# Performance work log

Measured on AMD Instinct MI355X. Metric: run time of the kernel, lower is better.

Reference implementation:

```python
import jax, jax.numpy as jnp
import numpy as np

B, DIM, NX, NY = 4, 64, 256, 256
HEADS, DIM_HEAD, LATENT, DIM_OUT, KM = 4, 32, 128, 64, 2
DH = DIM_HEAD * KM  # LowRankKernel head dim (also RoPE dim) = 64
EPS = 1e-5
MIN_FREQ = 1.0 / 64.0  # RotaryEmbedding default in FactFormer/LNS repo


def _gelu(x):
    return jax.nn.gelu(x, approximate=False)  # torch nn.GELU default (erf)


def _conv1x1(u, w):
    # u: [b,c,h,w], w: [out,c]  (1x1 conv == channel matmul)
    return jnp.einsum('bchw,oc->bohw', u, w)


def _pooling_reducer(x, win, ln_g, ln_b, w1, w2, b2):
    # x: [b, n_keep, n_pool, c] -> Linear, mean-pool over n_pool, LN+FFN
    h = jnp.einsum('bnmc,hc->bnmh', x, win).mean(axis=2)  # [b, n, hid]
    m = h.mean(axis=-1, keepdims=True)
    v = h.var(axis=-1, keepdims=True)
    h = (h - m) / jnp.sqrt(v + EPS) * ln_g + ln_b
    return _gelu(h @ w1.T) @ w2.T + b2  # [b, n, latent]


def _rope_freqs(n):
    pos = jnp.linspace(0.0, 1.0, n) / MIN_FREQ  # scale/min_freq = 64
    inv = 1.0 / (10000.0 ** (jnp.arange(0, DH, 2, dtype=jnp.float32) / DH))
    f = pos[:, None] * inv[None, :]            # [n, DH//2]
    return jnp.concatenate([f, f], axis=-1)    # [n, DH]


def _apply_rope(x, f):
    # rotate_half = cat(-x2, x1) on half-split (FactFormer convention)
    d = x.shape[-1] // 2
    rot = jnp.concatenate([-x[..., d:], x[..., :d]], axis=-1)
    return x * jnp.cos(f) + rot * jnp.sin(f)


def _low_rank_kernel(x, wqk):
    # x: [b, n, latent] -> K: [b, heads, n, n]; scaling=1, dropout=Identity, qk_norm=False
    b, n, _ = x.shape
    qk = x @ wqk.T
    q, k = jnp.split(qk, 2, axis=-1)
    q = q.reshape(b, n, HEADS, DH).transpose(0, 2, 1, 3)
    k = k.reshape(b, n, HEADS, DH).transpose(0, 2, 1, 3)
    f = _rope_freqs(n)
    q = _apply_rope(q, f)
    k = _apply_rope(k, f)
    return jnp.einsum('bhid,bhjd->bhij', q, k)


def _forward(u, gn_w, gn_b, w_in_proj, w_to_in,
             px_win, px_ln_g, px_ln_b, px_w1, px_w2, px_b2,
             py_win, py_ln_g, py_ln_b, py_w1, py_w2, py_b2,
             kx_wqk, ky_wqk, out_w1, out_w2):
    # GroupNorm(1, dim): normalize over (C,H,W) per sample, affine
    m = u.mean(axis=(1, 2, 3), keepdims=True)
    v = u.var(axis=(1, 2, 3), keepdims=True)
    un = (u - m) / jnp.sqrt(v + EPS) * gn_w[None, :, None, None] + gn_b[None, :, None, None]
    u_phi = _conv1x1(un, w_in_proj)  # [b, heads*dim_head, nx, ny]
    ui = _conv1x1(un, w_to_in)       # [b, dim, nx, ny]
    # to_x: pool over ny -> tokens along nx; to_y: pool over nx -> tokens along ny
    ux = _pooling_reducer(ui.transpose(0, 2, 3, 1), px_win, px_ln_g, px_ln_b, px_w1, px_w2, px_b2)  # [b, nx, latent]
    uy = _pooling_reducer(ui.transpose(0, 3, 2, 1), py_win, py_ln_g, py_ln_b, py_w1, py_w2, py_b2)  # [b, ny, latent]
    kx = _low_rank_kernel(ux, kx_wqk)  # [b, h, nx, nx]
    ky = _low_rank_kernel(uy, ky_wqk)  # [b, h, ny, ny]
    b, hc, nx, ny = u_phi.shape
    up = u_phi.reshape(b, HEADS, hc // HEADS, nx, ny)
    up = jnp.einsum('bhij,bhcjm->bhcim', kx, up)
    up = jnp.einsum('bhlm,bhcim->bhcil', ky, up)
    up = up.reshape(b, hc, nx, ny)
    # InstanceNorm2d (no affine, no running stats)
    m2 = up.mean(axis=(2, 3), keepdims=True)
    v2 = up.var(axis=(2, 3), keepdims=True)
    upn = (up - m2) / jnp.sqrt(v2 + EPS)
    out = _conv1x1(_gelu(_conv1x1(upn, out_w1)), out_w2)
    return out + u


def setup_inputs() -> dict:
    key = jax.random.key(0)
    ks = jax.random.split(key, 16)
    def w(k, shape, s=0.02):
        return (jax.random.normal(k, shape) * s).astype(jnp.float32)
    return {
        'u': jax.random.normal(ks[0], (B, DIM, NX, NY), dtype=jnp.float32),
        'gn_w': jnp.ones((DIM,), jnp.float32), 'gn_b': jnp.zeros((DIM,), jnp.float32),
        'w_in_proj': w(ks[1], (HEADS * DIM_HEAD, DIM)),
        'w_to_in': w(ks[2], (DIM, DIM)),
        'px_win': w(ks[3], (DIM, DIM)),
        'px_ln_g': jnp.ones((DIM,), jnp.float32), 'px_ln_b': jnp.zeros((DIM,), jnp.float32),
        'px_w1': w(ks[4], (2 * DIM, DIM)), 'px_w2': w(ks[5], (LATENT, 2 * DIM)),
        'px_b2': jnp.zeros((LATENT,), jnp.float32),
        'py_win': w(ks[6], (DIM, DIM)),
        'py_ln_g': jnp.ones((DIM,), jnp.float32), 'py_ln_b': jnp.zeros((DIM,), jnp.float32),
        'py_w1': w(ks[7], (2 * DIM, DIM)), 'py_w2': w(ks[8], (LATENT, 2 * DIM)),
        'py_b2': jnp.zeros((LATENT,), jnp.float32),
        'kx_wqk': w(ks[9], (2 * HEADS * DH, LATENT)),
        'ky_wqk': w(ks[10], (2 * HEADS * DH, LATENT)),
        'out_w1': w(ks[11], (DIM_OUT, HEADS * DIM_HEAD)),
        'out_w2': w(ks[12], (DIM_OUT, DIM_OUT)),
    }


def reference(u, gn_w, gn_b, w_in_proj, w_to_in,
              px_win, px_ln_g, px_ln_b, px_w1, px_w2, px_b2,
              py_win, py_ln_g, py_ln_b, py_w1, py_w2, py_b2,
              kx_wqk, ky_wqk, out_w1, out_w2):
    return _forward(u, gn_w, gn_b, w_in_proj, w_to_in,
                    px_win, px_ln_g, px_ln_b, px_w1, px_w2, px_b2,
                    py_win, py_ln_g, py_ln_b, py_w1, py_w2, py_b2,
                    kx_wqk, ky_wqk, out_w1, out_w2)
```

## Files before the change

### kernel.cpp

```cpp
#include <hip/hip_runtime.h>
#include <math.h>

typedef unsigned short ushort_t;
typedef unsigned int uint_t;
typedef __attribute__((ext_vector_type(8))) short s8v;
typedef __attribute__((ext_vector_type(4))) float f4;

#define NPIX 65536
#define EPS_ 1e-5f

__device__ __forceinline__ float bf2f(ushort_t u){ return __uint_as_float(((uint_t)u)<<16); }
__device__ __forceinline__ ushort_t f2bf(float f){
  uint_t u = __float_as_uint(f);
  uint_t r = (u + 0x7fffu + ((u>>16)&1u)) >> 16;
  return (ushort_t)r;
}
__device__ __forceinline__ float bflo(uint_t p){ return __uint_as_float(p<<16); }
__device__ __forceinline__ float bfhi(uint_t p){ return __uint_as_float(p & 0xffff0000u); }
__device__ __forceinline__ uint_t packbf(float a, float b){ return (uint_t)f2bf(a) | ((uint_t)f2bf(b)<<16); }

__device__ __forceinline__ f4 MFMA(s8v a, s8v b, f4 c){
  return __builtin_amdgcn_mfma_f32_16x16x32_bf16(a, b, c, 0, 0, 0);
}

__device__ __forceinline__ float wave_sum(float v){
  #pragma unroll
  for(int m=32;m>=1;m>>=1) v += __shfl_xor(v, m, 64);
  return v;
}

__global__ __launch_bounds__(256) void k1_stats(const float* __restrict__ u,
    float* __restrict__ part, float* __restrict__ pc, float* __restrict__ poolx){
  int blk = blockIdx.x; int b = blk>>8; int c = (blk>>2)&63; int iq = blk&3;
  int t = threadIdx.x; int lane = t&63; int w = t>>6;
  const float* up = u + ((size_t)(b*64+c))*NPIX + iq*64*256;
  __shared__ float red[8];
  float cs=0.f, ss=0.f;
  for(int r=0;r<64;r++){
    float v = up[r*256 + t];
    cs += v; ss += v*v;
  }
  pc[((b*64+c)*4 + iq)*256 + t] = cs;
  float a1 = wave_sum(cs), a2 = wave_sum(ss);
  if(lane==0){ red[w]=a1; red[4+w]=a2; }
  __syncthreads();
  if(t==0){
    part[((b*64+c)*4+iq)*2]   = red[0]+red[1]+red[2]+red[3];
    part[((b*64+c)*4+iq)*2+1] = red[4]+red[5]+red[6]+red[7];
  }
  int r = t>>2, ck = t&3;
  const float* rp = up + r*256 + ck*64;
  float s=0.f;
  #pragma unroll 4
  for(int j=0;j<16;j++){
    float4 v4 = *(const float4*)(rp + j*4);
    s += v4.x + v4.y + v4.z + v4.w;
  }
  s += __shfl_xor(s, 1, 64);
  s += __shfl_xor(s, 2, 64);
  if(ck==0) poolx[(b*256 + iq*64 + r)*64 + c] = s * (1.f/256.f);
}

__global__ void k2_fin(const float* __restrict__ part, float* __restrict__ gnmv){
  int t = threadIdx.x; int b = t>>6; int i = t&63;
  float S1=0.f, S2=0.f;
  #pragma unroll
  for(int q=0;q<4;q++){
    S1 += part[((b*64+i)*4+q)*2];
    S2 += part[((b*64+i)*4+q)*2+1];
  }
  S1 = wave_sum(S1); S2 = wave_sum(S2);
  if(i==0){
    const float inv = 1.f/4194304.f;
    float m = S1*inv; float v = S2*inv - m*m;
    gnmv[b*2] = m; gnmv[b*2+1] = rsqrtf(v + EPS_);
  }
}

__global__ __launch_bounds__(256) void k2b_pool(const float* __restrict__ pc,
    float* __restrict__ pooly){
  int blk = blockIdx.x; int b = blk>>6; int c = blk&63;
  int t = threadIdx.x;
  const float* p = pc + ((size_t)(b*64+c))*4*256 + t;
  float s = p[0] + p[256] + p[512] + p[768];
  pooly[(b*256+t)*64 + c] = s * (1.f/256.f);
}

__global__ __launch_bounds__(256) void k8a_fold(const float* __restrict__ gnmv,
    const float* __restrict__ gnw, const float* __restrict__ gnb,
    const float* __restrict__ w_in_proj, const float* __restrict__ out_w2,
    ushort_t* __restrict__ wpb, float* __restrict__ c0g, ushort_t* __restrict__ w2b){
  int b = blockIdx.x; int t = threadIdx.x;
  __shared__ float scs[64], shs[64];
  if(t<64){
    float mean = gnmv[b*2], rstd = gnmv[b*2+1];
    float sc = rstd*gnw[t];
    scs[t] = sc; shs[t] = gnb[t] - mean*sc;
  }
  __syncthreads();
  int oc = t>>1, h = t&1;
  float c0 = 0.f;
  for(int k=0;k<32;k++){
    int ch = h*32 + k;
    float wv = w_in_proj[oc*64 + ch];
    wpb[((size_t)b*128 + oc)*64 + ch] = f2bf(wv*scs[ch]);
    c0 += wv*shs[ch];
  }
  c0 += __shfl_xor(c0, 1, 64);
  if(h==0) c0g[b*128 + oc] = c0;
  if(b==0){
    for(int e=t;e<4096;e+=256) w2b[e] = f2bf(out_w2[e]);
  }
}

__global__ void k8b_fold(const float* __restrict__ istat,
    const float* __restrict__ out_w1, ushort_t* __restrict__ W1b,
    float* __restrict__ bias1){
  int b = blockIdx.x; int t = threadIdx.x;
  __shared__ float ms[128], rss[128];
  ms[t] = istat[(b*128+t)*2];       rss[t] = istat[(b*128+t)*2+1];
  ms[64+t] = istat[(b*128+64+t)*2]; rss[64+t] = istat[(b*128+64+t)*2+1];
  __syncthreads();
  float bias = 0.f;
  for(int ch=0;ch<128;ch++){
    float wv = out_w1[t*128 + ch];
    float wr = wv*rss[ch];
    W1b[((size_t)b*64 + t)*128 + ch] = f2bf(wr);
    bias += wr*ms[ch];
  }
  bias1[b*64 + t] = bias;
}

__global__ __launch_bounds__(128) void k3_reduce(
    const float* __restrict__ poolx, const float* __restrict__ pooly,
    const float* __restrict__ gnmv,
    const float* __restrict__ gnw, const float* __restrict__ gnb,
    const float* __restrict__ w_to_in,
    const float* __restrict__ xwin, const float* __restrict__ xlg, const float* __restrict__ xlb,
    const float* __restrict__ xw1, const float* __restrict__ xw2, const float* __restrict__ xb2,
    const float* __restrict__ ywin, const float* __restrict__ ylg, const float* __restrict__ ylb,
    const float* __restrict__ yw1, const float* __restrict__ yw2, const float* __restrict__ yb2,
    float* __restrict__ ux, float* __restrict__ uy){
  int id = blockIdx.x;
  int side = id >> 10; int r = id & 1023; int b = r>>8; int i = r&255;
  const float* pool = side ? pooly : poolx;
  const float* win = side ? ywin : xwin;
  const float* lg  = side ? ylg  : xlg;
  const float* lb  = side ? ylb  : xlb;
  const float* w1  = side ? yw1  : xw1;
  const float* w2  = side ? yw2  : xw2;
  const float* b2  = side ? yb2  : xb2;
  float* outp = side ? uy : ux;
  int t = threadIdx.x;
  __shared__ float pn[64], t1[64], hh[64], f1[128];
  float mean = gnmv[b*2], rstd = gnmv[b*2+1];
  if(t<64){
    float pv = pool[(b*256+i)*64 + t];
    pn[t] = (pv - mean)*rstd*gnw[t] + gnb[t];
  }
  __syncthreads();
  if(t<64){
    float acc=0.f; const float* wr = w_to_in + t*64;
    #pragma unroll 8
    for(int c=0;c<64;c++) acc += pn[c]*wr[c];
    t1[t]=acc;
  }
  __syncthreads();
  if(t<64){
    float acc=0.f; const float* wr = win + t*64;
    #pragma unroll 8
    for(int c=0;c<64;c++) acc += t1[c]*wr[c];
    hh[t]=acc;
  }
  __syncthreads();
  if(t<64){
    float v = hh[t];
    float s = wave_sum(v);
    float ss = wave_sum(v*v);
    float m2 = s*(1.f/64.f);
    float var = ss*(1.f/64.f) - m2*m2;
    float rs2 = rsqrtf(var + EPS_);
    hh[t] = (v - m2)*rs2*lg[t] + lb[t];
  }
  __syncthreads();
  {
    float acc=0.f; const float* wr = w1 + t*64;
    #pragma unroll 8
    for(int c=0;c<64;c++) acc += hh[c]*wr[c];
    f1[t] = 0.5f*acc*(1.f + erff(acc*0.70710678118654752f));
  }
  __syncthreads();
  {
    float acc=0.f; const float* wr = w2 + t*128;
    #pragma unroll 8
    for(int j=0;j<128;j++) acc += f1[j]*wr[j];
    outp[(b*256+i)*128 + t] = acc + b2[t];
  }
}

__global__ __launch_bounds__(256) void k4_gemm(
    const float* __restrict__ ux, const float* __restrict__ uy,
    const float* __restrict__ wqkx, const float* __restrict__ wqky,
    ushort_t* __restrict__ qxb, ushort_t* __restrict__ kxTb,
    ushort_t* __restrict__ qyb, ushort_t* __restrict__ kyTb){
  int blk = blockIdx.x;
  int nt = blk&3; int mt = (blk>>2)&1; int b = (blk>>3)&3; int side = blk>>5;
  const float* x  = (side? uy:ux) + (size_t)(b*256 + mt*128)*128;
  const float* wq = (side? wqky:wqkx) + (size_t)nt*128*128;
  ushort_t* qb  = side? qyb : qxb;
  ushort_t* kTb = side? kyTb : kxTb;

  __shared__ __align__(16) ushort_t sA[128*136];
  __shared__ __align__(16) ushort_t sB[128*136];

  int t = threadIdx.x; int lane = t&63; int w = t>>6; int lr = lane&15; int lg = lane>>4;
  for(int e=t;e<4096;e+=256){
    int row = e>>5, c4 = (e&31)*4;
    float4 v = *(const float4*)(x + row*128 + c4);
    uint2 pk; pk.x = packbf(v.x,v.y); pk.y = packbf(v.z,v.w);
    *(uint2*)&sA[row*136 + c4] = pk;
    float4 wv = *(const float4*)(wq + row*128 + c4);
    uint2 wk; wk.x = packbf(wv.x,wv.y); wk.y = packbf(wv.z,wv.w);
    *(uint2*)&sB[row*136 + c4] = wk;
  }
  __syncthreads();
  const f4 fz = {0.f,0.f,0.f,0.f};
  f4 acc[2][8];
  #pragma unroll
  for(int it=0;it<2;it++)
    #pragma unroll
    for(int n2=0;n2<8;n2++) acc[it][n2]=fz;
  #pragma unroll
  for(int kc=0;kc<4;kc++){
    s8v bf[8];
    #pragma unroll
    for(int n2=0;n2<8;n2++)
      bf[n2] = *(const s8v*)&sB[(n2*16+lr)*136 + kc*32 + lg*8];
    #pragma unroll
    for(int it=0;it<2;it++){
      s8v a = *(const s8v*)&sA[(w*32+it*16+lr)*136 + kc*32 + lg*8];
      #pragma unroll
      for(int n2=0;n2<8;n2++)
        acc[it][n2] = MFMA(a, bf[n2], acc[it][n2]);
    }
  }
  if(nt < 2){
    #pragma unroll
    for(int it=0;it<2;it++){
      #pragma unroll
      for(int n2=0;n2<8;n2++){
        int o = nt*128 + n2*16 + lr;
        int h = o>>6, dd = o&63, t32 = dd&31;
        float invf = expf(-(float)t32*(9.210340371976184f/32.f));
        size_t base = (size_t)(b*4+h)*16384;
        #pragma unroll
        for(int r=0;r<4;r++){
          int i = mt*128 + w*32 + it*16 + lg*4 + r;
          float f = (64.f/255.f)*(float)i*invf;
          float sn, cs; __sincosf(f, &sn, &cs);
          float pair = acc[it][n2^2][r];
          float rot = ((n2&2)==0)? -pair : pair;
          float v = acc[it][n2][r]*cs + rot*sn;
          qb[base + (size_t)i*64 + dd] = f2bf(v);
        }
      }
    }
  } else {
    __syncthreads();
    #pragma unroll
    for(int it=0;it<2;it++){
      #pragma unroll
      for(int n2=0;n2<8;n2++){
        int ol = n2*16 + lr;
        int o = nt*128 + ol;
        int t32 = o&31;
        float invf = expf(-(float)t32*(9.210340371976184f/32.f));
        #pragma unroll
        for(int r=0;r<4;r++){
          int il = w*32 + it*16 + lg*4 + r;
          int i = mt*128 + il;
          float f = (64.f/255.f)*(float)i*invf;
          float sn, cs; __sincosf(f, &sn, &cs);
          float pair = acc[it][n2^2][r];
          float rot = ((n2&2)==0)? -pair : pair;
          float v = acc[it][n2][r]*cs + rot*sn;
          sA[ol*136 + il] = f2bf(v);
        }
      }
    }
    __syncthreads();
    {
      int row = t>>1, half = t&1;
      int h = (nt-2)*2 + (row>>6), dd = row&63;
      ushort_t* dst = kTb + (size_t)(b*4+h)*16384 + (size_t)dd*256 + mt*128 + half*64;
      const ushort_t* src = &sA[row*136 + half*64];
      #pragma unroll
      for(int j=0;j<8;j++)
        *(uint4*)(dst + j*8) = *(const uint4*)(src + j*8);
    }
  }
}

__global__ __launch_bounds__(256) void k5s_sums(const ushort_t* __restrict__ kxTb,
    const ushort_t* __restrict__ kyTb, float* __restrict__ ksum){
  int bh = blockIdx.x; int t = threadIdx.x;
  int row = t>>2, g = t&3;
  const ushort_t* kx = kxTb + (size_t)bh*16384 + row*256 + g*64;
  float s = 0.f;
  #pragma unroll
  for(int j=0;j<8;j++){
    uint4 v = *(const uint4*)(kx + j*8);
    s += bflo(v.x)+bfhi(v.x)+bflo(v.y)+bfhi(v.y)+bflo(v.z)+bfhi(v.z)+bflo(v.w)+bfhi(v.w);
  }
  s += __shfl_xor(s,1,64); s += __shfl_xor(s,2,64);
  if(g==0) ksum[bh*128 + row] = s;
  const ushort_t* ky = kyTb + (size_t)bh*16384 + row*256 + g*64;
  float s2 = 0.f;
  #pragma unroll
  for(int j=0;j<8;j++){
    uint4 v = *(const uint4*)(ky + j*8);
    s2 += bflo(v.x)+bfhi(v.x)+bflo(v.y)+bfhi(v.y)+bflo(v.z)+bfhi(v.z)+bflo(v.w)+bfhi(v.w);
  }
  s2 += __shfl_xor(s2,1,64); s2 += __shfl_xor(s2,2,64);
  if(g==0) ksum[bh*128 + 64 + row] = s2;
}

__global__ __launch_bounds__(512) void k7a_core(
    const float* __restrict__ u,
    const ushort_t* __restrict__ kxTb, const ushort_t* __restrict__ kyTb,
    ushort_t* __restrict__ Cb){
  int blk = blockIdx.x; int b = blk>>6;
  const float* up = u + (size_t)blk*NPIX;
  __shared__ __align__(16) ushort_t su[2][64*264];
  __shared__ __align__(16) ushort_t sT1[4][64*68];
  int t = threadIdx.x; int w = t>>6; int lane = t&63; int lr = lane&15; int lg = lane>>4;
  int h = w>>1, sub = w&1;
  const ushort_t* KyT = kyTb + (size_t)(b*4+h)*16384;
  const ushort_t* KxT = kxTb + (size_t)(b*4+h)*16384;
  const f4 fz = {0.f,0.f,0.f,0.f};
  f4 cacc[2][4];
  #pragma unroll
  for(int it=0;it<2;it++)
    #pragma unroll
    for(int et=0;et<4;et++) cacc[it][et]=fz;

  auto stageld = [&](int jc, int buf){
    #pragma unroll
    for(int k=0;k<8;k++){
      int flat = k*512 + t;
      int row = flat>>6, col4 = flat&63;
      float4 v = *(const float4*)(up + (size_t)(jc*64+row)*256 + col4*4);
      uint2 pk; pk.x = packbf(v.x,v.y); pk.y = packbf(v.z,v.w);
      *(uint2*)&su[buf][row*264 + col4*4] = pk;
    }
  };
  stageld(0, 0);
  __syncthreads();
  for(int jc=0;jc<4;jc++){
    int cur = jc&1;
    f4 acc[2][4];
    #pragma unroll
    for(int jt=0;jt<2;jt++)
      #pragma unroll
      for(int et=0;et<4;et++) acc[jt][et]=fz;
    #pragma unroll
    for(int km=0;km<8;km++){
      s8v a0 = *(const s8v*)&su[cur][(sub*32+lr)*264 + km*32 + lg*8];
      s8v a1 = *(const s8v*)&su[cur][(sub*32+16+lr)*264 + km*32 + lg*8];
      #pragma unroll
      for(int et=0;et<4;et++){
        s8v bv = *(const s8v*)(KyT + (et*16+lr)*256 + km*32 + lg*8);
        acc[0][et] = MFMA(a0,bv,acc[0][et]);
        acc[1][et] = MFMA(a1,bv,acc[1][et]);
      }
    }
    #pragma unroll
    for(int jt=0;jt<2;jt++)
      #pragma unroll
      for(int et=0;et<4;et++){
        f4 v = acc[jt][et];
        uint2 pk; pk.x=packbf(v.x,v.y); pk.y=packbf(v.z,v.w);
        *(uint2*)&sT1[h][(et*16+lr)*68 + sub*32 + jt*16 + lg*4] = pk;
      }
    __syncthreads();
    if(jc<3) stageld(jc+1, cur^1);
    #pragma unroll
    for(int kj=0;kj<2;kj++){
      s8v a0 = *(const s8v*)(KxT + (size_t)(sub*32+lr)*256 + jc*64 + kj*32 + lg*8);
      s8v a1 = *(const s8v*)(KxT + (size_t)(sub*32+16+lr)*256 + jc*64 + kj*32 + lg*8);
      #pragma unroll
      for(int et=0;et<4;et++){
        s8v bv = *(const s8v*)&sT1[h][(et*16+lr)*68 + kj*32 + lg*8];
        cacc[0][et] = MFMA(a0,bv,cacc[0][et]);
        cacc[1][et] = MFMA(a1,bv,cacc[1][et]);
      }
    }
    __syncthreads();
  }
  ushort_t* cbase = Cb + ((size_t)blk*4 + h)*4096;
  #pragma unroll
  for(int it=0;it<2;it++)
    #pragma unroll
    for(int et=0;et<4;et++){
      f4 v = cacc[it][et];
      uint2 pk; pk.x=packbf(v.x,v.y); pk.y=packbf(v.z,v.w);
      *(uint2*)&cbase[(et*16+lr)*64 + sub*32 + it*16 + lg*4] = pk;
    }
}

__global__ __launch_bounds__(256) void k7m_mix(
    const ushort_t* __restrict__ Cb, const ushort_t* __restrict__ wpb,
    const float* __restrict__ c0g, const float* __restrict__ ksum,
    ushort_t* __restrict__ cT){
  int blk = blockIdx.x; int bh = blk>>4; int et = blk&15;
  int b = bh>>2, h = bh&3;
  __shared__ __align__(16) ushort_t sC[64*264];
  __shared__ float sWf[32*64];
  __shared__ float sKx[64], sKy4[4];
  int t = threadIdx.x;
  #pragma unroll
  for(int k=0;k<8;k++){
    int flat = k*256 + t;
    int ic = flat>>5, q = flat&31;
    uint4 v = *(const uint4*)(Cb + ((size_t)(b*64+ic)*4 + h)*4096 + et*256 + q*8);
    *(uint4*)&sC[ic*264 + q*8] = v;
  }
  for(int e=t;e<2048;e+=256){
    int ch = e>>6, ic = e&63;
    sWf[e] = bf2f(wpb[((size_t)b*128 + h*32 + ch)*64 + ic]);
  }
  if(t<64) sKx[t] = ksum[bh*128 + t];
  if(t<4)  sKy4[t] = ksum[bh*128 + 64 + et*4 + t];
  __syncthreads();
  int chg = t>>5, edq = t&31, ed0 = edq*8;
  float c0v[4];
  #pragma unroll
  for(int cc=0;cc<4;cc++) c0v[cc] = c0g[b*128 + h*32 + chg*4 + cc];
  float acc[4][8];
  #pragma unroll
  for(int j=0;j<8;j++){
    int ed = ed0 + j;
    float r1 = sKy4[ed>>6]*sKx[ed&63];
    #pragma unroll
    for(int cc=0;cc<4;cc++) acc[cc][j] = c0v[cc]*r1;
  }
  for(int ic=0;ic<64;ic++){
    uint4 cv = *(const uint4*)&sC[ic*264 + ed0];
    float x[8];
    x[0]=bflo(cv.x); x[1]=bfhi(cv.x); x[2]=bflo(cv.y); x[3]=bfhi(cv.y);
    x[4]=bflo(cv.z); x[5]=bfhi(cv.z); x[6]=bflo(cv.w); x[7]=bfhi(cv.w);
    #pragma unroll
    for(int cc=0;cc<4;cc++){
      float wv = sWf[(chg*4+cc)*64 + ic];
      #pragma unroll
      for(int j=0;j<8;j++) acc[cc][j] += wv*x[j];
    }
  }
  #pragma unroll
  for(int cc=0;cc<4;cc++){
    uint2 p0, p1;
    p0.x = packbf(acc[cc][0],acc[cc][1]); p0.y = packbf(acc[cc][2],acc[cc][3]);
    p1.x = packbf(acc[cc][4],acc[cc][5]); p1.y = packbf(acc[cc][6],acc[cc][7]);
    ushort_t* dst = cT + ((size_t)bh*32 + chg*4+cc)*4096 + et*256 + ed0;
    *(uint2*)(dst) = p0;
    *(uint2*)(dst+4) = p1;
  }
}

__global__ __launch_bounds__(256) void k7b_heavy(
    const ushort_t* __restrict__ cT,
    const ushort_t* __restrict__ qxb, const ushort_t* __restrict__ qyb,
    ushort_t* __restrict__ up2, float* __restrict__ istat){
  int blk = blockIdx.x;
  int c = blk & 31; int h = (blk>>5)&3; int b = blk>>7;
  int bh = b*4 + h; int ch = h*32 + c;
  const ushort_t* Qx  = qxb + (size_t)bh*16384;
  const ushort_t* Qy  = qyb + (size_t)bh*16384;
  const ushort_t* cTc = cT + (size_t)(bh*32 + c)*4096;
  ushort_t* out_c = up2 + (size_t)(b*128 + ch)*NPIX;

  __shared__ __align__(16) ushort_t sP[256*72];
  __shared__ float sRed[8];

  int t = threadIdx.x; int w = t>>6; int lane = t&63; int lr = lane&15; int lg = lane>>4;
  const f4 fz = {0.f,0.f,0.f,0.f};
  {
    s8v aF[4][2];
    #pragma unroll
    for(int me=0;me<4;me++)
      #pragma unroll
      for(int kd=0;kd<2;kd++)
        aF[me][kd] = *(const s8v*)(cTc + (me*16+lr)*64 + kd*32 + lg*8);
    #pragma unroll
    for(int it=0;it<4;it++){
      s8v b0 = *(const s8v*)(Qx + (w*64+it*16+lr)*64 + lg*8);
      s8v b1 = *(const s8v*)(Qx + (w*64+it*16+lr)*64 + 32 + lg*8);
      #pragma unroll
      for(int me=0;me<4;me++){
        f4 pv = MFMA(aF[me][0], b0, fz);
        pv = MFMA(aF[me][1], b1, pv);
        uint2 pk; pk.x=packbf(pv.x,pv.y); pk.y=packbf(pv.z,pv.w);
        *(uint2*)&sP[(w*64+it*16+lr)*72 + me*16 + lg*4] = pk;
      }
    }
  }
  __syncthreads();
  float lsum=0.f, lssq=0.f;
  {
    s8v aP[4][2];
    #pragma unroll
    for(int it=0;it<4;it++)
      #pragma unroll
      for(int ke=0;ke<2;ke++)
        aP[it][ke] = *(const s8v*)&sP[(w*64+it*16+lr)*72 + ke*32 + lg*8];
    for(int lt=0;lt<4;lt++){
      s8v bq[4][2];
      #pragma unroll
      for(int nt=0;nt<4;nt++)
        #pragma unroll
        for(int ke=0;ke<2;ke++)
          bq[nt][ke] = *(const s8v*)(Qy + (lt*64+nt*16+lr)*64 + ke*32 + lg*8);
      #pragma unroll
      for(int it=0;it<4;it++){
        #pragma unroll
        for(int nt=0;nt<4;nt++){
          f4 o = MFMA(bq[nt][0], aP[it][0], fz);
          o = MFMA(bq[nt][1], aP[it][1], o);
          lsum += o[0]+o[1]+o[2]+o[3];
          lssq += o[0]*o[0]+o[1]*o[1]+o[2]*o[2]+o[3]*o[3];
          uint2 pk; pk.x = packbf(o[0],o[1]); pk.y = packbf(o[2],o[3]);
          *(uint2*)(out_c + (size_t)(w*64 + it*16 + lr)*256 + lt*64 + nt*16 + lg*4) = pk;
        }
      }
    }
  }
  float a1 = wave_sum(lsum), a2 = wave_sum(lssq);
  if(lane==0){ sRed[w]=a1; sRed[4+w]=a2; }
  __syncthreads();
  if(t==0){
    float S = sRed[0]+sRed[1]+sRed[2]+sRed[3];
    float SS = sRed[4]+sRed[5]+sRed[6]+sRed[7];
    float m = S*(1.f/65536.f);
    float var = SS*(1.f/65536.f) - m*m;
    istat[(b*128+ch)*2] = m;
    istat[(b*128+ch)*2+1] = rsqrtf(var + EPS_);
  }
}

__global__ __launch_bounds__(256) void kf_out(
    const ushort_t* __restrict__ up2, const ushort_t* __restrict__ W1b,
    const float* __restrict__ bias1, const ushort_t* __restrict__ w2b,
    const float* __restrict__ u, float* __restrict__ out){
  int blk = blockIdx.x;
  int b = blk>>9; int pix0 = (blk&511)<<7;
  __shared__ __align__(16) unsigned char smraw[128*132*2];
  ushort_t* sX = (ushort_t*)smraw;
  ushort_t* sG = (ushort_t*)smraw;
  float* sO = (float*)smraw;
  int t = threadIdx.x; int lane = t&63; int w = t>>6; int lr = lane&15; int lg = lane>>4;
  {
    int ch = t>>4; int px = (t&15)*8;
    #pragma unroll
    for(int it=0; it<8; it++){
      int c = it*16 + ch;
      uint4 v = *(const uint4*)(up2 + ((size_t)(b*128+c))*NPIX + pix0 + px);
      uint2 lo; lo.x = v.x; lo.y = v.y;
      uint2 hi; hi.x = v.z; hi.y = v.w;
      *(uint2*)&sX[c*132 + px] = lo;
      *(uint2*)&sX[c*132 + px + 4] = hi;
    }
  }
  __syncthreads();
  const ushort_t* w1p = W1b + (size_t)b*64*128;
  f4 g[2][4];
  #pragma unroll
  for(int it=0;it<2;it++)
    #pragma unroll
    for(int nt=0;nt<4;nt++){
      float bv = -bias1[b*64 + nt*16 + lr];
      f4 ci = {bv,bv,bv,bv};
      g[it][nt] = ci;
    }
  #pragma unroll
  for(int kc=0;kc<4;kc++){
    s8v bf[4];
    #pragma unroll
    for(int nt=0;nt<4;nt++)
      bf[nt] = *(const s8v*)(w1p + (nt*16+lr)*128 + kc*32 + lg*8);
    #pragma unroll
    for(int it=0;it<2;it++){
      int pix = w*32 + it*16 + lr;
      s8v a;
      #pragma unroll
      for(int j=0;j<8;j++) a[j] = (short)sX[(kc*32+lg*8+j)*132 + pix];
      #pragma unroll
      for(int nt=0;nt<4;nt++)
        g[it][nt] = MFMA(a, bf[nt], g[it][nt]);
    }
  }
  #pragma unroll
  for(int it=0;it<2;it++)
    #pragma unroll
    for(int nt=0;nt<4;nt++){
      f4 v = g[it][nt];
      #pragma unroll
      for(int r=0;r<4;r++){
        float x = v[r];
        v[r] = 0.5f*x*(1.f + erff(x*0.70710678118654752f));
      }
      g[it][nt] = v;
    }
  __syncthreads();
  #pragma unroll
  for(int it=0;it<2;it++)
    #pragma unroll
    for(int nt=0;nt<4;nt++){
      f4 v = g[it][nt];
      uint2 pk; pk.x = packbf(v.x,v.y); pk.y = packbf(v.z,v.w);
      *(uint2*)&sG[(nt*16+lr)*132 + w*32 + it*16 + lg*4] = pk;
    }
  __syncthreads();
  f4 o2[2][4];
  const f4 fz = {0.f,0.f,0.f,0.f};
  #pragma unroll
  for(int it=0;it<2;it++)
    #pragma unroll
    for(int nt=0;nt<4;nt++) o2[it][nt]=fz;
  #pragma unroll
  for(int kc=0;kc<2;kc++){
    s8v bf[4];
    #pragma unroll
    for(int nt=0;nt<4;nt++)
      bf[nt] = *(const s8v*)(w2b + (nt*16+lr)*64 + kc*32 + lg*8);
    #pragma unroll
    for(int it=0;it<2;it++){
      int pix = w*32 + it*16 + lr;
      s8v a;
      #pragma unroll
      for(int j=0;j<8;j++) a[j] = (short)sG[(kc*32+lg*8+j)*132 + pix];
      #pragma unroll
      for(int nt=0;nt<4;nt++)
        o2[it][nt] = MFMA(a, bf[nt], o2[it][nt]);
    }
  }
  __syncthreads();
  #pragma unroll
  for(int it=0;it<2;it++)
    #pragma unroll
    for(int nt=0;nt<4;nt++)
      *(f4*)&sO[(nt*16+lr)*132 + w*32 + it*16 + lg*4] = o2[it][nt];
  __syncthreads();
  {
    int oc = t>>5; int px = (t&31)*4;
    #pragma unroll
    for(int it=0;it<8;it++){
      int o = it*8 + oc;
      float4 ov = *(const float4*)&sO[o*132 + px];
      float4 uv = *(const float4*)(u + ((size_t)(b*64+o))*NPIX + pix0 + px);
      float4 rv;
      rv.x = ov.x+uv.x; rv.y = ov.y+uv.y; rv.z = ov.z+uv.z; rv.w = ov.w+uv.w;
      *(float4*)(out + ((size_t)(b*64+o))*NPIX + pix0 + px) = rv;
    }
  }
}

extern "C" void kernel_launch(void* const* d_in, const int* in_sizes, int n_in,
                              void* d_out, int out_size, void* d_ws, size_t ws_size,
                              hipStream_t stream) {
  (void)in_sizes; (void)n_in; (void)out_size; (void)ws_size;
  const float* u        = (const float*)d_in[0];
  const float* gnw      = (const float*)d_in[1];
  const float* gnb      = (const float*)d_in[2];
  const float* w_in_proj= (const float*)d_in[3];
  const float* w_to_in  = (const float*)d_in[4];
  const float* px_win   = (const float*)d_in[5];
  const float* px_ln_g  = (const float*)d_in[6];
  const float* px_ln_b  = (const float*)d_in[7];
  const float* px_w1    = (const float*)d_in[8];
  const float* px_w2    = (const float*)d_in[9];
  const float* px_b2    = (const float*)d_in[10];
  const float* py_win   = (const float*)d_in[11];
  const float* py_ln_g  = (const float*)d_in[12];
  const float* py_ln_b  = (const float*)d_in[13];
  const float* py_w1    = (const float*)d_in[14];
  const float* py_w2    = (const float*)d_in[15];
  const float* py_b2    = (const float*)d_in[16];
  const float* kx_wqk   = (const float*)d_in[17];
  const float* ky_wqk   = (const float*)d_in[18];
  const float* out_w1   = (const float*)d_in[19];
  const float* out_w2   = (const float*)d_in[20];
  float* out = (float*)d_out;

  float* fw = (float*)d_ws;
  float* part  = fw + 0;
  float* gnmv  = fw + 2048;
  float* pc    = fw + 4096;
  float* poolx = fw + 266240;
  float* pooly = fw + 331776;
  float* ux    = fw + 397312;
  float* uy    = fw + 528384;
  float* istat = fw + 659456;
  float* c0g   = fw + 660480;
  float* bias1 = fw + 660992;
  ushort_t* wpb = (ushort_t*)(fw + 661504);
  ushort_t* W1b = (ushort_t*)(fw + 677888);
  ushort_t* w2b = (ushort_t*)(fw + 694272);
  float* ksum   = fw + 696320;
  ushort_t* qxb  = (ushort_t*)(fw + 4096);
  ushort_t* kxTb = (ushort_t*)(fw + 135168);
  ushort_t* qyb  = (ushort_t*)(fw + 698368);
  ushort_t* kyTb = (ushort_t*)(fw + 829440);
  ushort_t* up2  = (ushort_t*)(fw + 960512);
  ushort_t* Cb = (ushort_t*)d_out;
  ushort_t* cT = (ushort_t*)d_out + 4194304;

  k1_stats<<<dim3(1024), dim3(256), 0, stream>>>(u, part, pc, poolx);
  k2_fin<<<dim3(1), dim3(256), 0, stream>>>(part, gnmv);
  k2b_pool<<<dim3(256), dim3(256), 0, stream>>>(pc, pooly);
  k8a_fold<<<dim3(4), dim3(256), 0, stream>>>(gnmv, gnw, gnb, w_in_proj, out_w2, wpb, c0g, w2b);
  k3_reduce<<<dim3(2048), dim3(128), 0, stream>>>(poolx, pooly, gnmv, gnw, gnb, w_to_in,
      px_win, px_ln_g, px_ln_b, px_w1, px_w2, px_b2,
      py_win, py_ln_g, py_ln_b, py_w1, py_w2, py_b2, ux, uy);
  k4_gemm<<<dim3(64), dim3(256), 0, stream>>>(ux, uy, kx_wqk, ky_wqk, qxb, kxTb, qyb, kyTb);
  k5s_sums<<<dim3(16), dim3(256), 0, stream>>>(kxTb, kyTb, ksum);
  k7a_core<<<dim3(256), dim3(512), 0, stream>>>(u, kxTb, kyTb, Cb);
  k7m_mix<<<dim3(256), dim3(256), 0, stream>>>(Cb, wpb, c0g, ksum, cT);
  k7b_heavy<<<dim3(512), dim3(256), 0, stream>>>(cT, qxb, qyb, up2, istat);
  k8b_fold<<<dim3(4), dim3(64), 0, stream>>>(istat, out_w1, W1b, bias1);
  kf_out<<<dim3(2048), dim3(256), 0, stream>>>(up2, W1b, bias1, w2b, u, out);
}
```

Baseline: 210.5 us.

## Split core kernel over row halves, fuse pooling into stats, drop k2b_pool

k1_stats now reads each row once as float4 per wave, computing the row pool sums, column sums and sum of squares in that single pass instead of re-reading the tile for x-pooling. The k2b_pool kernel is removed; k3_reduce computes y-pool values directly from the column partials. k7a_core is split into two blocks per (batch, channel), each covering half of the rows with a single-buffered stage, which doubles the grid to 512 blocks. Its two partial outputs are summed inside k7m_mix, which now reads Cb directly from global memory instead of staging it in LDS. The cost is twice the Cb storage and traffic, plus the loss of the double-buffered load overlap in k7a_core.

Measured after the change: 217.8 us. +3.4%, slower.

```diff
diff --git a/kernel.cpp b/kernel.cpp
--- a/kernel.cpp
+++ b/kernel.cpp
@@ -34,31 +34,32 @@
   int blk = blockIdx.x; int b = blk>>8; int c = (blk>>2)&63; int iq = blk&3;
   int t = threadIdx.x; int lane = t&63; int w = t>>6;
   const float* up = u + ((size_t)(b*64+c))*NPIX + iq*64*256;
+  __shared__ float sCol[4][256];
   __shared__ float red[8];
-  float cs=0.f, ss=0.f;
-  for(int r=0;r<64;r++){
-    float v = up[r*256 + t];
-    cs += v; ss += v*v;
-  }
-  pc[((b*64+c)*4 + iq)*256 + t] = cs;
-  float a1 = wave_sum(cs), a2 = wave_sum(ss);
-  if(lane==0){ red[w]=a1; red[4+w]=a2; }
+  float4 cs4 = {0.f,0.f,0.f,0.f};
+  float ss = 0.f;
+  #pragma unroll 4
+  for(int r16=0;r16<16;r16++){
+    int r = w*16 + r16;
+    float4 v = *(const float4*)(up + r*256 + lane*4);
+    cs4.x+=v.x; cs4.y+=v.y; cs4.z+=v.z; cs4.w+=v.w;
+    ss += v.x*v.x+v.y*v.y+v.z*v.z+v.w*v.w;
+    float rs = wave_sum(v.x+v.y+v.z+v.w);
+    if(lane==0) poolx[(b*256 + iq*64 + r)*64 + c] = rs*(1.f/256.f);
+  }
+  *(float4*)&sCol[w][lane*4] = cs4;
+  float ssw = wave_sum(ss);
+  if(lane==0) red[w] = ssw;
+  __syncthreads();
+  float colsum = sCol[0][t]+sCol[1][t]+sCol[2][t]+sCol[3][t];
+  pc[((b*64+c)*4+iq)*256 + t] = colsum;
+  float s1 = wave_sum(colsum);
+  if(lane==0) red[4+w] = s1;
   __syncthreads();
   if(t==0){
-    part[((b*64+c)*4+iq)*2]   = red[0]+red[1]+red[2]+red[3];
-    part[((b*64+c)*4+iq)*2+1] = red[4]+red[5]+red[6]+red[7];
-  }
-  int r = t>>2, ck = t&3;
-  const float* rp = up + r*256 + ck*64;
-  float s=0.f;
-  #pragma unroll 4
-  for(int j=0;j<16;j++){
-    float4 v4 = *(const float4*)(rp + j*4);
-    s += v4.x + v4.y + v4.z + v4.w;
-  }
-  s += __shfl_xor(s, 1, 64);
-  s += __shfl_xor(s, 2, 64);
-  if(ck==0) poolx[(b*256 + iq*64 + r)*64 + c] = s * (1.f/256.f);
+    part[((b*64+c)*4+iq)*2]   = red[4]+red[5]+red[6]+red[7];
+    part[((b*64+c)*4+iq)*2+1] = red[0]+red[1]+red[2]+red[3];
+  }
 }
 
 __global__ void k2_fin(const float* __restrict__ part, float* __restrict__ gnmv){
@@ -75,15 +76,6 @@
     float m = S1*inv; float v = S2*inv - m*m;
     gnmv[b*2] = m; gnmv[b*2+1] = rsqrtf(v + EPS_);
   }
-}
-
-__global__ __launch_bounds__(256) void k2b_pool(const float* __restrict__ pc,
-    float* __restrict__ pooly){
-  int blk = blockIdx.x; int b = blk>>6; int c = blk&63;
-  int t = threadIdx.x;
-  const float* p = pc + ((size_t)(b*64+c))*4*256 + t;
-  float s = p[0] + p[256] + p[512] + p[768];
-  pooly[(b*256+t)*64 + c] = s * (1.f/256.f);
 }
 
 __global__ __launch_bounds__(256) void k8a_fold(const float* __restrict__ gnmv,
@@ -132,7 +124,7 @@
 }
 
 __global__ __launch_bounds__(128) void k3_reduce(
-    const float* __restrict__ poolx, const float* __restrict__ pooly,
+    const float* __restrict__ poolx, const float* __restrict__ pc,
     const float* __restrict__ gnmv,
     const float* __restrict__ gnw, const float* __restrict__ gnb,
     const float* __restrict__ w_to_in,
@@ -143,7 +135,6 @@
     float* __restrict__ ux, float* __restrict__ uy){
   int id = blockIdx.x;
   int side = id >> 10; int r = id & 1023; int b = r>>8; int i = r&255;
-  const float* pool = side ? pooly : poolx;
   const float* win = side ? ywin : xwin;
   const float* lg  = side ? ylg  : xlg;
   const float* lb  = side ? ylb  : xlb;
@@ -155,7 +146,13 @@
   __shared__ float pn[64], t1[64], hh[64], f1[128];
   float mean = gnmv[b*2], rstd = gnmv[b*2+1];
   if(t<64){
-    float pv = pool[(b*256+i)*64 + t];
+    float pv;
+    if(side){
+      const float* p = pc + ((size_t)(b*64+t)*4)*256 + i;
+      pv = (p[0] + p[256] + p[512] + p[768]) * (1.f/256.f);
+    } else {
+      pv = poolx[(b*256+i)*64 + t];
+    }
     pn[t] = (pv - mean)*rstd*gnw[t] + gnb[t];
   }
   __syncthreads();
@@ -329,9 +326,9 @@
     const float* __restrict__ u,
     const ushort_t* __restrict__ kxTb, const ushort_t* __restrict__ kyTb,
     ushort_t* __restrict__ Cb){
-  int blk = blockIdx.x; int b = blk>>6;
-  const float* up = u + (size_t)blk*NPIX;
-  __shared__ __align__(16) ushort_t su[2][64*264];
+  int blk = blockIdx.x; int b = blk>>7; int ch = (blk>>1)&63; int half = blk&1;
+  const float* up = u + (size_t)(b*64+ch)*NPIX;
+  __shared__ __align__(16) ushort_t su[64*264];
   __shared__ __align__(16) ushort_t sT1[4][64*68];
   int t = threadIdx.x; int w = t>>6; int lane = t&63; int lr = lane&15; int lg = lane>>4;
   int h = w>>1, sub = w&1;
@@ -344,20 +341,17 @@
     #pragma unroll
     for(int et=0;et<4;et++) cacc[it][et]=fz;
 
-  auto stageld = [&](int jc, int buf){
+  for(int jcl=0;jcl<2;jcl++){
+    int jc = half*2 + jcl;
     #pragma unroll
     for(int k=0;k<8;k++){
       int flat = k*512 + t;
       int row = flat>>6, col4 = flat&63;
       float4 v = *(const float4*)(up + (size_t)(jc*64+row)*256 + col4*4);
       uint2 pk; pk.x = packbf(v.x,v.y); pk.y = packbf(v.z,v.w);
-      *(uint2*)&su[buf][row*264 + col4*4] = pk;
-    }
-  };
-  stageld(0, 0);
-  __syncthreads();
-  for(int jc=0;jc<4;jc++){
-    int cur = jc&1;
+      *(uint2*)&su[row*264 + col4*4] = pk;
+    }
+    __syncthreads();
     f4 acc[2][4];
     #pragma unroll
     for(int jt=0;jt<2;jt++)
@@ -365,8 +359,8 @@
       for(int et=0;et<4;et++) acc[jt][et]=fz;
     #pragma unroll
     for(int km=0;km<8;km++){
-      s8v a0 = *(const s8v*)&su[cur][(sub*32+lr)*264 + km*32 + lg*8];
-      s8v a1 = *(const s8v*)&su[cur][(sub*32+16+lr)*264 + km*32 + lg*8];
+      s8v a0 = *(const s8v*)&su[(sub*32+lr)*264 + km*32 + lg*8];
+      s8v a1 = *(const s8v*)&su[(sub*32+16+lr)*264 + km*32 + lg*8];
       #pragma unroll
       for(int et=0;et<4;et++){
         s8v bv = *(const s8v*)(KyT + (et*16+lr)*256 + km*32 + lg*8);
@@ -383,7 +377,6 @@
         *(uint2*)&sT1[h][(et*16+lr)*68 + sub*32 + jt*16 + lg*4] = pk;
       }
     __syncthreads();
-    if(jc<3) stageld(jc+1, cur^1);
     #pragma unroll
     for(int kj=0;kj<2;kj++){
       s8v a0 = *(const s8v*)(KxT + (size_t)(sub*32+lr)*256 + jc*64 + kj*32 + lg*8);
@@ -395,7 +388,6 @@
         cacc[1][et] = MFMA(a1,bv,cacc[1][et]);
       }
     }
-    __syncthreads();
   }
   ushort_t* cbase = Cb + ((size_t)blk*4 + h)*4096;
   #pragma unroll
@@ -414,17 +406,9 @@
     ushort_t* __restrict__ cT){
   int blk = blockIdx.x; int bh = blk>>4; int et = blk&15;
   int b = bh>>2, h = bh&3;
-  __shared__ __align__(16) ushort_t sC[64*264];
   __shared__ float sWf[32*64];
   __shared__ float sKx[64], sKy4[4];
   int t = threadIdx.x;
-  #pragma unroll
-  for(int k=0;k<8;k++){
-    int flat = k*256 + t;
-    int ic = flat>>5, q = flat&31;
-    uint4 v = *(const uint4*)(Cb + ((size_t)(b*64+ic)*4 + h)*4096 + et*256 + q*8);
-    *(uint4*)&sC[ic*264 + q*8] = v;
-  }
   for(int e=t;e<2048;e+=256){
     int ch = e>>6, ic = e&63;
     sWf[e] = bf2f(wpb[((size_t)b*128 + h*32 + ch)*64 + ic]);
@@ -445,10 +429,14 @@
     for(int cc=0;cc<4;cc++) acc[cc][j] = c0v[cc]*r1;
   }
   for(int ic=0;ic<64;ic++){
-    uint4 cv = *(const uint4*)&sC[ic*264 + ed0];
+    const ushort_t* p = Cb + ((((size_t)(b*64+ic))*2)*4 + h)*4096 + et*256 + ed0;
+    uint4 v0 = *(const uint4*)p;
+    uint4 v1 = *(const uint4*)(p + 16384);
     float x[8];
-    x[0]=bflo(cv.x); x[1]=bfhi(cv.x); x[2]=bflo(cv.y); x[3]=bfhi(cv.y);
-    x[4]=bflo(cv.z); x[5]=bfhi(cv.z); x[6]=bflo(cv.w); x[7]=bfhi(cv.w);
+    x[0]=bflo(v0.x)+bflo(v1.x); x[1]=bfhi(v0.x)+bfhi(v1.x);
+    x[2]=bflo(v0.y)+bflo(v1.y); x[3]=bfhi(v0.y)+bfhi(v1.y);
+    x[4]=bflo(v0.z)+bflo(v1.z); x[5]=bfhi(v0.z)+bfhi(v1.z);
+    x[6]=bflo(v0.w)+bflo(v1.w); x[7]=bfhi(v0.w)+bfhi(v1.w);
     #pragma unroll
     for(int cc=0;cc<4;cc++){
       float wv = sWf[(chg*4+cc)*64 + ic];
@@ -696,7 +684,6 @@
   float* gnmv  = fw + 2048;
   float* pc    = fw + 4096;
   float* poolx = fw + 266240;
-  float* pooly = fw + 331776;
   float* ux    = fw + 397312;
   float* uy    = fw + 528384;
   float* istat = fw + 659456;
@@ -712,18 +699,17 @@
   ushort_t* kyTb = (ushort_t*)(fw + 829440);
   ushort_t* up2  = (ushort_t*)(fw + 960512);
   ushort_t* Cb = (ushort_t*)d_out;
-  ushort_t* cT = (ushort_t*)d_out + 4194304;
+  ushort_t* cT = (ushort_t*)d_out + 8388608;
 
   k1_stats<<<dim3(1024), dim3(256), 0, stream>>>(u, part, pc, poolx);
   k2_fin<<<dim3(1), dim3(256), 0, stream>>>(part, gnmv);
-  k2b_pool<<<dim3(256), dim3(256), 0, stream>>>(pc, pooly);
   k8a_fold<<<dim3(4), dim3(256), 0, stream>>>(gnmv, gnw, gnb, w_in_proj, out_w2, wpb, c0g, w2b);
-  k3_reduce<<<dim3(2048), dim3(128), 0, stream>>>(poolx, pooly, gnmv, gnw, gnb, w_to_in,
+  k3_reduce<<<dim3(2048), dim3(128), 0, stream>>>(poolx, pc, gnmv, gnw, gnb, w_to_in,
       px_win, px_ln_g, px_ln_b, px_w1, px_w2, px_b2,
       py_win, py_ln_g, py_ln_b, py_w1, py_w2, py_b2, ux, uy);
   k4_gemm<<<dim3(64), dim3(256), 0, stream>>>(ux, uy, kx_wqk, ky_wqk, qxb, kxTb, qyb, kyTb);
   k5s_sums<<<dim3(16), dim3(256), 0, stream>>>(kxTb, kyTb, ksum);
-  k7a_core<<<dim3(256), dim3(512), 0, stream>>>(u, kxTb, kyTb, Cb);
+  k7a_core<<<dim3(512), dim3(512), 0, stream>>>(u, kxTb, kyTb, Cb);
   k7m_mix<<<dim3(256), dim3(256), 0, stream>>>(Cb, wpb, c0g, ksum, cT);
   k7b_heavy<<<dim3(512), dim3(256), 0, stream>>>(cT, qxb, qyb, up2, istat);
   k8b_fold<<<dim3(4), dim3(64), 0, stream>>>(istat, out_w1, W1b, bias1);
```

## Compute instance-norm stats via Qy Gram matrix and fuse final Qy expansion into output

Applied to the files above, without the earlier changes.

Instead of materializing the full 128-channel x 65536-pixel intermediate (up2) in k7b and reading it back in kf_out, k7p now writes only the small rank-64 factor P per channel. It computes mean and variance algebraically from a precomputed Qy Gram matrix and Qy column sums (new k5g_gram kernel, with k4 also writing a transposed Qy). kf_out re-expands P·Qy^T per tile with MFMA before the output MLP. This cuts a large bf16 round trip through global memory in exchange for recomputing the expansion in kf_out, an extra small kernel, and variance computed as E[x²]-m² from bf16-rounded factors.

Measured after the change: 229.5 us. 9.0% more time.

```diff
diff --git a/kernel.cpp b/kernel.cpp
--- a/kernel.cpp
+++ b/kernel.cpp
@@ -202,7 +202,8 @@
     const float* __restrict__ ux, const float* __restrict__ uy,
     const float* __restrict__ wqkx, const float* __restrict__ wqky,
     ushort_t* __restrict__ qxb, ushort_t* __restrict__ kxTb,
-    ushort_t* __restrict__ qyb, ushort_t* __restrict__ kyTb){
+    ushort_t* __restrict__ qyb, ushort_t* __restrict__ kyTb,
+    ushort_t* __restrict__ qyTb){
   int blk = blockIdx.x;
   int nt = blk&3; int mt = (blk>>2)&1; int b = (blk>>3)&3; int side = blk>>5;
   const float* x  = (side? uy:ux) + (size_t)(b*256 + mt*128)*128;
@@ -264,6 +265,38 @@
           qb[base + (size_t)i*64 + dd] = f2bf(v);
         }
       }
+    }
+    if(side==1){
+      __syncthreads();
+      #pragma unroll
+      for(int it=0;it<2;it++){
+        #pragma unroll
+        for(int n2=0;n2<8;n2++){
+          int ol = n2*16 + lr;
+          int o = nt*128 + ol;
+          int t32 = o&31;
+          float invf = expf(-(float)t32*(9.210340371976184f/32.f));
+          #pragma unroll
+          for(int r=0;r<4;r++){
+            int il = w*32 + it*16 + lg*4 + r;
+            int i = mt*128 + il;
+            float f = (64.f/255.f)*(float)i*invf;
+            float sn, cs; __sincosf(f, &sn, &cs);
+            float pair = acc[it][n2^2][r];
+            float rot = ((n2&2)==0)? -pair : pair;
+            float v = acc[it][n2][r]*cs + rot*sn;
+            sA[ol*136 + il] = f2bf(v);
+          }
+        }
+      }
+      __syncthreads();
+      int row = t>>1, half = t&1;
+      int h = nt*2 + (row>>6), dd = row&63;
+      ushort_t* dst = qyTb + (size_t)(b*4+h)*16384 + (size_t)dd*256 + mt*128 + half*64;
+      const ushort_t* src = &sA[row*136 + half*64];
+      #pragma unroll
+      for(int j=0;j<8;j++)
+        *(uint4*)(dst + j*8) = *(const uint4*)(src + j*8);
     }
   } else {
     __syncthreads();
@@ -325,6 +358,43 @@
   if(g==0) ksum[bh*128 + 64 + row] = s2;
 }
 
+__global__ __launch_bounds__(256) void k5g_gram(const ushort_t* __restrict__ qyTb,
+    ushort_t* __restrict__ Gyb, float* __restrict__ qysg){
+  int bh = blockIdx.x; int t = threadIdx.x;
+  int lane = t&63; int w = t>>6; int lr = lane&15; int lg = lane>>4;
+  const ushort_t* qT = qyTb + (size_t)bh*16384;
+  {
+    int e = t>>2, g = t&3;
+    const ushort_t* p = qT + e*256 + g*64;
+    float s = 0.f;
+    #pragma unroll
+    for(int j=0;j<8;j++){
+      uint4 v = *(const uint4*)(p + j*8);
+      s += bflo(v.x)+bfhi(v.x)+bflo(v.y)+bfhi(v.y)+bflo(v.z)+bfhi(v.z)+bflo(v.w)+bfhi(v.w);
+    }
+    s += __shfl_xor(s,1,64); s += __shfl_xor(s,2,64);
+    if(g==0) qysg[bh*64 + e] = s;
+  }
+  const f4 fz = {0.f,0.f,0.f,0.f};
+  f4 acc[4];
+  #pragma unroll
+  for(int n=0;n<4;n++) acc[n]=fz;
+  #pragma unroll
+  for(int kc=0;kc<8;kc++){
+    s8v am = *(const s8v*)(qT + (w*16+lr)*256 + kc*32 + lg*8);
+    #pragma unroll
+    for(int n=0;n<4;n++){
+      s8v bn = *(const s8v*)(qT + (n*16+lr)*256 + kc*32 + lg*8);
+      acc[n] = MFMA(am, bn, acc[n]);
+    }
+  }
+  #pragma unroll
+  for(int n=0;n<4;n++)
+    #pragma unroll
+    for(int r=0;r<4;r++)
+      Gyb[(size_t)bh*4096 + (n*16+lr)*64 + w*16 + lg*4 + r] = f2bf(acc[n][r]);
+}
+
 __global__ __launch_bounds__(512) void k7a_core(
     const float* __restrict__ u,
     const ushort_t* __restrict__ kxTb, const ushort_t* __restrict__ kyTb,
@@ -467,23 +537,27 @@
   }
 }
 
-__global__ __launch_bounds__(256) void k7b_heavy(
+__global__ __launch_bounds__(256) void k7p_core(
     const ushort_t* __restrict__ cT,
-    const ushort_t* __restrict__ qxb, const ushort_t* __restrict__ qyb,
-    ushort_t* __restrict__ up2, float* __restrict__ istat){
+    const ushort_t* __restrict__ qxb, const ushort_t* __restrict__ Gyb,
+    const float* __restrict__ qysg,
+    ushort_t* __restrict__ Pbuf, float* __restrict__ istat){
   int blk = blockIdx.x;
   int c = blk & 31; int h = (blk>>5)&3; int b = blk>>7;
   int bh = b*4 + h; int ch = h*32 + c;
   const ushort_t* Qx  = qxb + (size_t)bh*16384;
-  const ushort_t* Qy  = qyb + (size_t)bh*16384;
   const ushort_t* cTc = cT + (size_t)(bh*32 + c)*4096;
-  ushort_t* out_c = up2 + (size_t)(b*128 + ch)*NPIX;
+  const ushort_t* Gyp = Gyb + (size_t)bh*4096;
 
   __shared__ __align__(16) ushort_t sP[256*72];
+  __shared__ float sQys[64];
   __shared__ float sRed[8];
 
   int t = threadIdx.x; int w = t>>6; int lane = t&63; int lr = lane&15; int lg = lane>>4;
+  if(t<64) sQys[t] = qysg[bh*64 + t];
+  __syncthreads();
   const f4 fz = {0.f,0.f,0.f,0.f};
+  float msum = 0.f, ssum = 0.f;
   {
     s8v aF[4][2];
     #pragma unroll
@@ -499,13 +573,14 @@
       for(int me=0;me<4;me++){
         f4 pv = MFMA(aF[me][0], b0, fz);
         pv = MFMA(aF[me][1], b1, pv);
+        int e0 = me*16 + lg*4;
+        msum += pv[0]*sQys[e0] + pv[1]*sQys[e0+1] + pv[2]*sQys[e0+2] + pv[3]*sQys[e0+3];
         uint2 pk; pk.x=packbf(pv.x,pv.y); pk.y=packbf(pv.z,pv.w);
-        *(uint2*)&sP[(w*64+it*16+lr)*72 + me*16 + lg*4] = pk;
-      }
-    }
-  }
-  __syncthreads();
-  float lsum=0.f, lssq=0.f;
+        *(uint2*)&sP[(w*64+it*16+lr)*72 + e0] = pk;
+      }
+    }
+  }
+  __syncthreads();
   {
     s8v aP[4][2];
     #pragma unroll
@@ -513,61 +588,76 @@
       #pragma unroll
       for(int ke=0;ke<2;ke++)
         aP[it][ke] = *(const s8v*)&sP[(w*64+it*16+lr)*72 + ke*32 + lg*8];
-    for(int lt=0;lt<4;lt++){
-      s8v bq[4][2];
-      #pragma unroll
-      for(int nt=0;nt<4;nt++)
+    #pragma unroll
+    for(int nf=0;nf<4;nf++){
+      s8v bg0 = *(const s8v*)(Gyp + (nf*16+lr)*64 + lg*8);
+      s8v bg1 = *(const s8v*)(Gyp + (nf*16+lr)*64 + 32 + lg*8);
+      #pragma unroll
+      for(int it=0;it<4;it++){
+        f4 rv = MFMA(aP[it][0], bg0, fz);
+        rv = MFMA(aP[it][1], bg1, rv);
         #pragma unroll
-        for(int ke=0;ke<2;ke++)
-          bq[nt][ke] = *(const s8v*)(Qy + (lt*64+nt*16+lr)*64 + ke*32 + lg*8);
-      #pragma unroll
-      for(int it=0;it<4;it++){
-        #pragma unroll
-        for(int nt=0;nt<4;nt++){
-          f4 o = MFMA(bq[nt][0], aP[it][0], fz);
-          o = MFMA(bq[nt][1], aP[it][1], o);
-          lsum += o[0]+o[1]+o[2]+o[3];
-          lssq += o[0]*o[0]+o[1]*o[1]+o[2]*o[2]+o[3]*o[3];
-          uint2 pk; pk.x = packbf(o[0],o[1]); pk.y = packbf(o[2],o[3]);
-          *(uint2*)(out_c + (size_t)(w*64 + it*16 + lr)*256 + lt*64 + nt*16 + lg*4) = pk;
-        }
-      }
-    }
-  }
-  float a1 = wave_sum(lsum), a2 = wave_sum(lssq);
+        for(int r=0;r<4;r++)
+          ssum += rv[r] * bf2f(sP[(size_t)(w*64+it*16+lg*4+r)*72 + nf*16 + lr]);
+      }
+    }
+  }
+  {
+    const ushort_t* src = &sP[t*72];
+    ushort_t* dst = Pbuf + (((size_t)(b*256) + t)*128 + ch)*64;
+    #pragma unroll
+    for(int j=0;j<8;j++)
+      *(uint4*)(dst + j*8) = *(const uint4*)(src + j*8);
+  }
+  float a1 = wave_sum(msum), a2 = wave_sum(ssum);
   if(lane==0){ sRed[w]=a1; sRed[4+w]=a2; }
   __syncthreads();
   if(t==0){
-    float S = sRed[0]+sRed[1]+sRed[2]+sRed[3];
-    float SS = sRed[4]+sRed[5]+sRed[6]+sRed[7];
-    float m = S*(1.f/65536.f);
-    float var = SS*(1.f/65536.f) - m*m;
-    istat[(b*128+ch)*2] = m;
-    istat[(b*128+ch)*2+1] = rsqrtf(var + EPS_);
+    float M = (sRed[0]+sRed[1]+sRed[2]+sRed[3])*(1.f/65536.f);
+    float S = (sRed[4]+sRed[5]+sRed[6]+sRed[7])*(1.f/65536.f);
+    istat[(b*128+ch)*2] = M;
+    istat[(b*128+ch)*2+1] = rsqrtf(S - M*M + EPS_);
   }
 }
 
 __global__ __launch_bounds__(256) void kf_out(
-    const ushort_t* __restrict__ up2, const ushort_t* __restrict__ W1b,
-    const float* __restrict__ bias1, const ushort_t* __restrict__ w2b,
-    const float* __restrict__ u, float* __restrict__ out){
+    const ushort_t* __restrict__ Pbuf, const ushort_t* __restrict__ qyb,
+    const ushort_t* __restrict__ W1b, const float* __restrict__ bias1,
+    const ushort_t* __restrict__ w2b, const float* __restrict__ u,
+    float* __restrict__ out){
   int blk = blockIdx.x;
   int b = blk>>9; int pix0 = (blk&511)<<7;
-  __shared__ __align__(16) unsigned char smraw[128*132*2];
-  ushort_t* sX = (ushort_t*)smraw;
+  int irow = pix0>>8; int l0 = pix0&255;
+  __shared__ __align__(16) unsigned char smraw[128*136*2];
+  ushort_t* sX2 = (ushort_t*)smraw;
   ushort_t* sG = (ushort_t*)smraw;
   float* sO = (float*)smraw;
   int t = threadIdx.x; int lane = t&63; int w = t>>6; int lr = lane&15; int lg = lane>>4;
+  const f4 fz = {0.f,0.f,0.f,0.f};
   {
-    int ch = t>>4; int px = (t&15)*8;
-    #pragma unroll
-    for(int it=0; it<8; it++){
-      int c = it*16 + ch;
-      uint4 v = *(const uint4*)(up2 + ((size_t)(b*128+c))*NPIX + pix0 + px);
-      uint2 lo; lo.x = v.x; lo.y = v.y;
-      uint2 hi; hi.x = v.z; hi.y = v.w;
-      *(uint2*)&sX[c*132 + px] = lo;
-      *(uint2*)&sX[c*132 + px + 4] = hi;
+    const ushort_t* Pi = Pbuf + ((size_t)(b*256 + irow))*128*64;
+    #pragma unroll
+    for(int h=0;h<4;h++){
+      const ushort_t* Qy = qyb + (size_t)(b*4+h)*16384;
+      s8v bq[2][2];
+      #pragma unroll
+      for(int lf=0;lf<2;lf++){
+        bq[lf][0] = *(const s8v*)(Qy + (l0 + w*32 + lf*16 + lr)*64 + lg*8);
+        bq[lf][1] = *(const s8v*)(Qy + (l0 + w*32 + lf*16 + lr)*64 + 32 + lg*8);
+      }
+      #pragma unroll
+      for(int cf=0;cf<2;cf++){
+        int chf = h*2 + cf;
+        s8v ap0 = *(const s8v*)(Pi + (chf*16+lr)*64 + lg*8);
+        s8v ap1 = *(const s8v*)(Pi + (chf*16+lr)*64 + 32 + lg*8);
+        #pragma unroll
+        for(int lf=0;lf<2;lf++){
+          f4 d = MFMA(ap0, bq[lf][0], fz);
+          d = MFMA(ap1, bq[lf][1], d);
+          uint2 pk; pk.x = packbf(d[0],d[1]); pk.y = packbf(d[2],d[3]);
+          *(uint2*)&sX2[(w*32 + lf*16 + lr)*136 + chf*16 + lg*4] = pk;
+        }
+      }
     }
   }
   __syncthreads();
@@ -590,9 +680,7 @@
     #pragma unroll
     for(int it=0;it<2;it++){
       int pix = w*32 + it*16 + lr;
-      s8v a;
-      #pragma unroll
-      for(int j=0;j<8;j++) a[j] = (short)sX[(kc*32+lg*8+j)*132 + pix];
+      s8v a = *(const s8v*)&sX2[pix*136 + kc*32 + lg*8];
       #pragma unroll
       for(int nt=0;nt<4;nt++)
         g[it][nt] = MFMA(a, bf[nt], g[it][nt]);
@@ -621,7 +709,6 @@
     }
   __syncthreads();
   f4 o2[2][4];
-  const f4 fz = {0.f,0.f,0.f,0.f};
   #pragma unroll
   for(int it=0;it<2;it++)
     #pragma unroll
@@ -710,7 +797,10 @@
   ushort_t* kxTb = (ushort_t*)(fw + 135168);
   ushort_t* qyb  = (ushort_t*)(fw + 698368);
   ushort_t* kyTb = (ushort_t*)(fw + 829440);
-  ushort_t* up2  = (ushort_t*)(fw + 960512);
+  ushort_t* qyTb = (ushort_t*)(fw + 960512);
+  ushort_t* Gyb  = (ushort_t*)(fw + 1091584);
+  float*    qysg = fw + 1124352;
+  ushort_t* Pbuf = (ushort_t*)(fw + 1125376);
   ushort_t* Cb = (ushort_t*)d_out;
   ushort_t* cT = (ushort_t*)d_out + 4194304;
 
@@ -721,11 +811,12 @@
   k3_reduce<<<dim3(2048), dim3(128), 0, stream>>>(poolx, pooly, gnmv, gnw, gnb, w_to_in,
       px_win, px_ln_g, px_ln_b, px_w1, px_w2, px_b2,
       py_win, py_ln_g, py_ln_b, py_w1, py_w2, py_b2, ux, uy);
-  k4_gemm<<<dim3(64), dim3(256), 0, stream>>>(ux, uy, kx_wqk, ky_wqk, qxb, kxTb, qyb, kyTb);
+  k4_gemm<<<dim3(64), dim3(256), 0, stream>>>(ux, uy, kx_wqk, ky_wqk, qxb, kxTb, qyb, kyTb, qyTb);
   k5s_sums<<<dim3(16), dim3(256), 0, stream>>>(kxTb, kyTb, ksum);
+  k5g_gram<<<dim3(16), dim3(256), 0, stream>>>(qyTb, Gyb, qysg);
   k7a_core<<<dim3(256), dim3(512), 0, stream>>>(u, kxTb, kyTb, Cb);
   k7m_mix<<<dim3(256), dim3(256), 0, stream>>>(Cb, wpb, c0g, ksum, cT);
-  k7b_heavy<<<dim3(512), dim3(256), 0, stream>>>(cT, qxb, qyb, up2, istat);
+  k7p_core<<<dim3(512), dim3(256), 0, stream>>>(cT, qxb, Gyb, qysg, Pbuf, istat);
   k8b_fold<<<dim3(4), dim3(64), 0, stream>>>(istat, out_w1, W1b, bias1);
-  kf_out<<<dim3(2048), dim3(256), 0, stream>>>(up2, W1b, bias1, w2b, u, out);
-}
+  kf_out<<<dim3(2048), dim3(256), 0, stream>>>(Pbuf, qyb, W1b, bias1, w2b, u, out);
+}
```
